# Performance work log

Measured on AMD Instinct MI355X. Metric: run time of the kernel, lower is better.

The kernel has to match this reference:

```python
import jax, jax.numpy as jnp
import numpy as np

K = 3
KK = K * K
PAD = 1          # kernel_size // 2
MAX_SHIFT = 8.0  # bias_range > 0
DEG = 2          # degrees = (2, 2), paon_type 'a'


def setup_inputs() -> dict:
    key = jax.random.key(0)
    ks = jax.random.split(key, 6)
    B, C, O, H, W = 4, 64, 64, 160, 160
    x = jax.random.normal(ks[0], (B, C, H, W), jnp.float32)
    # offset conv is 1x1: weight [2*K*K, C], bias [2*K*K]
    off_w = jax.random.normal(ks[1], (2 * KK, C), jnp.float32) * 0.1
    off_b = jax.random.normal(ks[2], (2 * KK,), jnp.float32) * 0.1
    scale = 1.0 / np.sqrt(C * KK).astype(np.float32)
    w_m = jax.random.normal(ks[3], (DEG * O, C, K, K), jnp.float32) * scale
    w_n = jax.random.normal(ks[4], (DEG * O, C, K, K), jnp.float32) * scale
    w0 = jax.random.normal(ks[5], (O,), jnp.float32) * 0.1
    return {"x": x, "off_w": off_w, "off_b": off_b, "w_m": w_m, "w_n": w_n, "w0": w0}


def _bilinear_sample(x, py, px):
    """x: [B,C,H,W]; py,px: [B,KK,H,W] -> [B,C,KK,H,W]; zero outside bounds."""
    B, C, H, W = x.shape
    xf = x.reshape(B, C, H * W)
    y0 = jnp.floor(py)
    x0 = jnp.floor(px)
    wy = py - y0
    wx = px - x0
    y0i = y0.astype(jnp.int32)
    x0i = x0.astype(jnp.int32)
    out = jnp.zeros((B, C) + py.shape[1:], x.dtype)
    corners = ((0, 0, (1 - wy) * (1 - wx)), (0, 1, (1 - wy) * wx),
               (1, 0, wy * (1 - wx)), (1, 1, wy * wx))
    for dy, dx, wgt in corners:
        yy = y0i + dy
        xx = x0i + dx
        valid = (yy >= 0) & (yy < H) & (xx >= 0) & (xx < W)
        idx = jnp.clip(yy, 0, H - 1) * W + jnp.clip(xx, 0, W - 1)
        g = jax.vmap(lambda f, i: f[:, i])(xf, idx.reshape(B, -1))  # [B,C,KK*H*W]
        out = out + g.reshape(B, C, *py.shape[1:]) * (wgt * valid)[:, None]
    return out


def _after_poly_a(y, ch, o, take_abs):
    # channel reorder + groupwise sum, per PaLaBase.after_poly_a
    order = np.array([(k * ch) % (ch * o) + k // o for k in range(ch * o)])
    y = y[:, order].reshape(y.shape[0], ch, o, *y.shape[2:])
    return jnp.abs(y).sum(2) if take_abs else y.sum(2)


def reference(x, off_w, off_b, w_m, w_n, w0):
    B, C, H, W = x.shape
    O = w0.shape[0]
    # --- DeformOffset: 1x1 conv -> clamp to image -> tanh soft-limit ---
    off_r = jnp.einsum('bchw,oc->bohw', x, off_w) + off_b[None, :, None, None]
    gy = jnp.arange(H, dtype=x.dtype)[None, None, :, None]
    gx = jnp.arange(W, dtype=x.dtype)[None, None, None, :]
    oy = jnp.clip(off_r[:, 0::2], -gy, H - gy)  # [B,KK,H,W] (dy per kernel pos)
    ox = jnp.clip(off_r[:, 1::2], -gx, W - gx)  # [B,KK,H,W] (dx per kernel pos)
    soft = lambda o: jnp.where(jnp.abs(o) >= MAX_SHIFT,
                               MAX_SHIFT * jnp.tanh(o / MAX_SHIFT), o)
    oy, ox = soft(oy), soft(ox)
    # --- deformable sampling grid (stride=1, dilation=1, zero padding) ---
    kidx = jnp.arange(KK)
    kh = (kidx // K).astype(x.dtype)[None, :, None, None]
    kw = (kidx % K).astype(x.dtype)[None, :, None, None]
    base_y = (jnp.arange(H, dtype=x.dtype) - PAD)[None, None, :, None]
    base_x = (jnp.arange(W, dtype=x.dtype) - PAD)[None, None, None, :]
    py = base_y + kh + oy
    px = base_x + kw + ox
    samp = _bilinear_sample(x, py, px)  # [B,C,KK,H,W]
    # --- Pade numerator / denominator convs on the sampled tensor ---
    pm_raw = jnp.einsum('bckhw,ock->bohw', samp, w_m.reshape(DEG * O, C, KK))
    qn_raw = jnp.einsum('bckhw,ock->bohw', samp, w_n.reshape(DEG * O, C, KK))
    pm = _after_poly_a(pm_raw, O, DEG, take_abs=False)
    qn = _after_poly_a(qn_raw, O, DEG, take_abs=True)
    # prepare_for_div_a: (pm + w0, 1 + qn)
    return (pm + w0[None, :, None, None]) / (1.0 + qn)
```

## Files before the change

### kernel.cpp

```cpp
#include <hip/hip_runtime.h>
#include <hip/hip_bf16.h>
#include <hip/hip_fp16.h>

#define Hh 160
#define Ww 160
#define Cc 64
#define HWc 25600
#define Bb 4
#define AST 76

typedef __attribute__((ext_vector_type(8))) short short8;
typedef __attribute__((ext_vector_type(4))) float f32x4;

__device__ __forceinline__ unsigned short f2bf(float f) {
  unsigned int u = __float_as_uint(f);
  unsigned int r = u + 0x7FFFu + ((u >> 16) & 1u);
  return (unsigned short)(r >> 16);
}
__device__ __forceinline__ float bflo(unsigned int u) {
  return __uint_as_float(u << 16);
}
__device__ __forceinline__ float bfhi(unsigned int u) {
  return __uint_as_float(u & 0xffff0000u);
}

__global__ __launch_bounds__(256) void k_prep(
    const float* __restrict__ x, const float* __restrict__ wm,
    const float* __restrict__ wn, const float* __restrict__ ow,
    unsigned short* __restrict__ xT, unsigned short* __restrict__ bf) {
  if (blockIdx.x < 400) {
    __shared__ unsigned short s[64][260];
    int wg = blockIdx.x;
    int b = wg / 100;
    int pix0 = (wg % 100) * 256;
    int l = threadIdx.x & 63, wv = threadIdx.x >> 6;
    const float* xb = x + (size_t)b * Cc * HWc + pix0;
#pragma unroll
    for (int i = 0; i < 16; i++) {
      int c = i * 4 + wv;
      float4 v = *(const float4*)&xb[(size_t)c * HWc + l * 4];
      unsigned int d0 = (unsigned int)f2bf(v.x) | ((unsigned int)f2bf(v.y) << 16);
      unsigned int d1 = (unsigned int)f2bf(v.z) | ((unsigned int)f2bf(v.w) << 16);
      *(uint2*)&s[c][l * 4] = make_uint2(d0, d1);
    }
    __syncthreads();
    int p = threadIdx.x;
    unsigned int w[32];
#pragma unroll
    for (int j = 0; j < 32; j++) {
      unsigned int a = s[2 * j][p];
      unsigned int bb = s[2 * j + 1][p];
      w[j] = a | (bb << 16);
    }
    unsigned short* dst = xT + ((size_t)(b * HWc + pix0 + p)) * 64;
#pragma unroll
    for (int j = 0; j < 8; j++)
      ((uint4*)dst)[j] = make_uint4(w[4 * j], w[4 * j + 1], w[4 * j + 2], w[4 * j + 3]);
  } else {
    int i = (blockIdx.x - 400) * 256 + threadIdx.x;
    if (i < 9 * 2 * 12 * 64 * 8) {
      int j2 = i & 7;
      int lane = (i >> 3) & 63;
      int ntck = i >> 9;
      int nt = ntck % 12;
      int ck = ntck / 12;
      int kk = ck >> 1;
      int chunk = ck & 1;
      int n = nt * 16 + (lane & 15);
      int c = chunk * 32 + (lane >> 4) * 8 + j2;
      float v;
      if (n < 64)
        v = wm[(n * 64 + c) * 9 + kk] + wm[((n + 64) * 64 + c) * 9 + kk];
      else
        v = wn[((n - 64) * 64 + c) * 9 + kk];
      bf[i] = f2bf(v);
    } else if (i < 9 * 2 * 12 * 64 * 8 + 2 * 2 * 64 * 8) {
      int j = i - 9 * 2 * 12 * 64 * 8;
      int j2 = j & 7;
      int lane = (j >> 3) & 63;
      int rest = j >> 9;
      int ntile = rest & 1;
      int chunk = rest >> 1;
      int n = ntile * 16 + (lane & 15);
      int c = chunk * 32 + (lane >> 4) * 8 + j2;
      bf[i] = (n < 18) ? f2bf(ow[n * 64 + c]) : (unsigned short)0;
    }
  }
}

__device__ __forceinline__ void gather2(const char* __restrict__ gbase, uint4 D,
                                        int chB, uint4& c00, uint4& c01,
                                        uint4& c10, uint4& c11, float& w00,
                                        float& w01, float& w10, float& w11) {
  int bb = D.x + chB;
  int dxB = (int)(D.y & 0xffffu);
  int dyB = (int)(D.y >> 16);
  c00 = *(const uint4*)(gbase + bb);
  c01 = *(const uint4*)(gbase + bb + dxB);
  c10 = *(const uint4*)(gbase + bb + dyB);
  c11 = *(const uint4*)(gbase + bb + (dxB + dyB));
  float2 wA = __half22float2(*(const __half2*)&D.z);
  float2 wB = __half22float2(*(const __half2*)&D.w);
  w00 = wA.x; w01 = wA.y; w10 = wB.x; w11 = wB.y;
}

__device__ __forceinline__ void combine_write(unsigned short* Arow,
                                              const uint4& c00, const uint4& c01,
                                              const uint4& c10, const uint4& c11,
                                              float w00, float w01, float w10,
                                              float w11) {
  const unsigned int* a = (const unsigned int*)&c00;
  const unsigned int* b = (const unsigned int*)&c01;
  const unsigned int* c = (const unsigned int*)&c10;
  const unsigned int* d = (const unsigned int*)&c11;
  unsigned int o[4];
#pragma unroll
  for (int j = 0; j < 4; j++) {
    float lo = bflo(a[j]) * w00 + bflo(b[j]) * w01 + bflo(c[j]) * w10 +
               bflo(d[j]) * w11;
    float hi = bfhi(a[j]) * w00 + bfhi(b[j]) * w01 + bfhi(c[j]) * w10 +
               bfhi(d[j]) * w11;
    __hip_bfloat162 hh = __float22bfloat162_rn(make_float2(lo, hi));
    o[j] = *(unsigned int*)&hh;
  }
  *(uint4*)Arow = make_uint4(o[0], o[1], o[2], o[3]);
}

__global__ __launch_bounds__(256, 4) void k_main(
    const unsigned short* __restrict__ xT, const float* __restrict__ w0,
    const float* __restrict__ off_b, const unsigned short* __restrict__ bfrag,
    const unsigned short* __restrict__ obfrag, float* __restrict__ out) {
  __shared__ unsigned short A[2][64 * AST];
  __shared__ uint4 gdesc[576];
  float2* spy = (float2*)&A[0][0];
  const int tid = threadIdx.x;
  const int wg = blockIdx.x;
  const int band = wg & 7;
  const int local = wg >> 3;
  const int b = local / 50;
  const int pix0 = band * 3200 + (local % 50) * 64;
  const int wv = tid >> 6;
  const int l = tid & 63;
  const int lm = l & 15;
  const int quad = l >> 4;
  const int ch8 = l & 7;
  const int pr = l >> 3;
  const int chB = ch8 * 16;

  const unsigned short* xTb = xT + (size_t)b * HWc * 64;
  const char* gbase = (const char*)xTb;

  f32x4 acc[3][4];
  const f32x4 zero = {0.f, 0.f, 0.f, 0.f};
#pragma unroll
  for (int j = 0; j < 3; j++)
#pragma unroll
    for (int pt = 0; pt < 4; pt++) acc[j][pt] = zero;

  {
    f32x4 aO0 = zero, aO1 = zero;
    const unsigned short* xrow = xTb + (size_t)(pix0 + wv * 16 + lm) * 64;
#pragma unroll
    for (int chunk = 0; chunk < 2; chunk++) {
      short8 sb = *(const short8*)(xrow + chunk * 32 + quad * 8);
      short8 wf0 = *(const short8*)&obfrag[((chunk * 2 + 0) * 64 + l) * 8];
      short8 wf1 = *(const short8*)&obfrag[((chunk * 2 + 1) * 64 + l) * 8];
      aO0 = __builtin_amdgcn_mfma_f32_16x16x32_bf16(wf0, sb, aO0, 0, 0, 0);
      aO1 = __builtin_amdgcn_mfma_f32_16x16x32_bf16(wf1, sb, aO1, 0, 0, 0);
    }
    int pix = pix0 + wv * 16 + lm;
    int h = pix / Ww, w = pix % Ww;
    float fh = (float)h, fw = (float)w;
#pragma unroll
    for (int rr = 0; rr < 2; rr++) {
      int n = quad * 4 + 2 * rr;
      int kk = n >> 1;
      float oy = aO0[2 * rr] + off_b[n];
      float ox = aO0[2 * rr + 1] + off_b[n + 1];
      oy = fminf(fmaxf(oy, -fh), 160.0f - fh);
      ox = fminf(fmaxf(ox, -fw), 160.0f - fw);
      if (fabsf(oy) >= 8.0f) oy = 8.0f * tanhf(oy * 0.125f);
      if (fabsf(ox) >= 8.0f) ox = 8.0f * tanhf(ox * 0.125f);
      spy[kk * 64 + wv * 16 + lm] =
          make_float2(fh - 1.0f + (float)(kk / 3) + oy,
                      fw - 1.0f + (float)(kk % 3) + ox);
    }
    if (quad == 0) {
      float oy = aO1[0] + off_b[16];
      float ox = aO1[1] + off_b[17];
      oy = fminf(fmaxf(oy, -fh), 160.0f - fh);
      ox = fminf(fmaxf(ox, -fw), 160.0f - fw);
      if (fabsf(oy) >= 8.0f) oy = 8.0f * tanhf(oy * 0.125f);
      if (fabsf(ox) >= 8.0f) ox = 8.0f * tanhf(ox * 0.125f);
      spy[8 * 64 + wv * 16 + lm] =
          make_float2(fh + 1.0f + oy, fw + 1.0f + ox);
    }
  }
  __syncthreads();

  for (int e = tid; e < 576; e += 256) {
    float2 P = spy[e];
    float py = P.x, pxv = P.y;
    float y0f = floorf(py), x0f = floorf(pxv);
    float wy = py - y0f, wx = pxv - x0f;
    int y0 = (int)y0f, x0 = (int)x0f;
    float vy0 = (y0 >= 0 && y0 < Hh) ? 1.f : 0.f;
    float vy1 = (y0 >= -1 && y0 < Hh - 1) ? 1.f : 0.f;
    float vx0 = (x0 >= 0 && x0 < Ww) ? 1.f : 0.f;
    float vx1 = (x0 >= -1 && x0 < Ww - 1) ? 1.f : 0.f;
    int r0 = min(max(y0, 0), Hh - 1);
    int r1 = min(max(y0 + 1, 0), Hh - 1);
    int c0 = min(max(x0, 0), Ww - 1);
    int c1 = min(max(x0 + 1, 0), Ww - 1);
    float w00 = (1.f - wy) * (1.f - wx) * vy0 * vx0;
    float w01 = (1.f - wy) * wx * vy0 * vx1;
    float w10 = wy * (1.f - wx) * vy1 * vx0;
    float w11 = wy * wx * vy1 * vx1;
    uint4 D;
    D.x = (unsigned int)((r0 * Ww + c0) * 128);
    D.y = (unsigned int)((c1 - c0) * 128) |
          ((unsigned int)((r1 - r0) * Ww * 128) << 16);
    __half2 hA = __floats2half2_rn(w00, w01);
    __half2 hB = __floats2half2_rn(w10, w11);
    D.z = *(unsigned int*)&hA;
    D.w = *(unsigned int*)&hB;
    gdesc[e] = D;
  }
  __syncthreads();

#pragma unroll
  for (int i = 0; i < 2; i++) {
    int pl = wv * 16 + i * 8 + pr;
    uint4 c00, c01, c10, c11;
    float w00, w01, w10, w11;
    gather2(gbase, gdesc[pl], chB, c00, c01, c10, c11, w00, w01, w10, w11);
    combine_write(&A[0][pl * AST + ch8 * 8], c00, c01, c10, c11, w00, w01, w10,
                  w11);
  }
  __syncthreads();

  for (int kk = 0; kk < 9; kk++) {
    const int cur = kk & 1;
    if (kk < 8) {
      uint4 g00[2], g01[2], g10[2], g11[2];
      float W00[2], W01[2], W10[2], W11[2];
#pragma unroll
      for (int i = 0; i < 2; i++) {
        int pl = wv * 16 + i * 8 + pr;
        gather2(gbase, gdesc[(kk + 1) * 64 + pl], chB, g00[i], g01[i], g10[i],
                g11[i], W00[i], W01[i], W10[i], W11[i]);
      }
#pragma unroll
      for (int i = 0; i < 2; i++) {
        int pl = wv * 16 + i * 8 + pr;
        combine_write(&A[cur ^ 1][pl * AST + ch8 * 8], g00[i], g01[i], g10[i],
                      g11[i], W00[i], W01[i], W10[i], W11[i]);
      }
    }
#pragma unroll
    for (int chunk = 0; chunk < 2; chunk++) {
      short8 sfr[4];
#pragma unroll
      for (int pt = 0; pt < 4; pt++)
        sfr[pt] = *(const short8*)&A[cur][(pt * 16 + lm) * AST + chunk * 32 +
                                          quad * 8];
      short8 wfr[3];
#pragma unroll
      for (int j = 0; j < 3; j++) {
        int nt = j * 4 + wv;
        wfr[j] = *(const short8*)&bfrag[((size_t)((kk * 2 + chunk) * 12 + nt) *
                                            64 + l) * 8];
      }
#pragma unroll
      for (int j = 0; j < 3; j++)
#pragma unroll
        for (int pt = 0; pt < 4; pt++)
          acc[j][pt] = __builtin_amdgcn_mfma_f32_16x16x32_bf16(
              wfr[j], sfr[pt], acc[j][pt], 0, 0, 0);
    }
    __syncthreads();
  }

  float w0v[4];
#pragma unroll
  for (int r = 0; r < 4; r++) w0v[r] = w0[wv * 16 + quad * 4 + r];
  float* ob = out + (size_t)b * Cc * HWc + pix0;
#pragma unroll
  for (int pt = 0; pt < 4; pt++) {
#pragma unroll
    for (int r = 0; r < 4; r++) {
      int oc = wv * 16 + quad * 4 + r;
      float pm = acc[0][pt][r] + w0v[r];
      float qn = 1.0f + fabsf(acc[1][pt][r]) + fabsf(acc[2][pt][r]);
      ob[oc * HWc + pt * 16 + lm] = pm / qn;
    }
  }
}

extern "C" void kernel_launch(void* const* d_in, const int* in_sizes, int n_in,
                              void* d_out, int out_size, void* d_ws, size_t ws_size,
                              hipStream_t stream) {
  const float* x = (const float*)d_in[0];
  const float* off_w = (const float*)d_in[1];
  const float* off_b = (const float*)d_in[2];
  const float* w_m = (const float*)d_in[3];
  const float* w_n = (const float*)d_in[4];
  const float* w0 = (const float*)d_in[5];
  float* out = (float*)d_out;

  unsigned short* bfrag = (unsigned short*)d_ws;
  unsigned short* obfrag = (unsigned short*)((char*)d_ws + (size_t)221184);
  unsigned short* xT = (unsigned short*)((char*)d_ws + (size_t)225280);

  hipLaunchKernelGGL(k_prep, dim3(840), dim3(256), 0, stream, x, w_m, w_n,
                     off_w, xT, bfrag);
  hipLaunchKernelGGL(k_main, dim3(1600), dim3(256), 0, stream, xT, w0, off_b,
                     bfrag, obfrag, out);
}
```

Baseline: 133.6 us.

## Gather bilinear samples directly into MFMA fragments with single-wave blocks

Replaces the 4-wave workgroup, which staged bilinear-sampled tiles in double-buffered shared memory, with one-wave blocks covering 32 pixels. Each lane gathers and blends its own MFMA B-fragment straight from global memory into registers, and computes all 12 output tiles with 24 accumulators. This removes the shared-memory staging, bank traffic and per-tap barriers. In exchange each wave reloads the full weight fragments from global/L2 per block, the gather is no longer prefetched a step ahead, and register pressure rises.

```diff
diff --git a/kernel.cpp b/kernel.cpp
--- a/kernel.cpp
+++ b/kernel.cpp
@@ -7,7 +7,6 @@
 #define Cc 64
 #define HWc 25600
 #define Bb 4
-#define AST 76
 
 typedef __attribute__((ext_vector_type(8))) short short8;
 typedef __attribute__((ext_vector_type(4))) float f32x4;
@@ -88,78 +87,65 @@
   }
 }
 
-__device__ __forceinline__ void gather2(const char* __restrict__ gbase, uint4 D,
-                                        int chB, uint4& c00, uint4& c01,
-                                        uint4& c10, uint4& c11, float& w00,
-                                        float& w01, float& w10, float& w11) {
-  int bb = D.x + chB;
+__device__ __forceinline__ short8 gcomb(const char* __restrict__ gbase, uint4 D,
+                                        int off) {
+  int bb = (int)D.x + off;
   int dxB = (int)(D.y & 0xffffu);
   int dyB = (int)(D.y >> 16);
-  c00 = *(const uint4*)(gbase + bb);
-  c01 = *(const uint4*)(gbase + bb + dxB);
-  c10 = *(const uint4*)(gbase + bb + dyB);
-  c11 = *(const uint4*)(gbase + bb + (dxB + dyB));
+  uint4 c00 = *(const uint4*)(gbase + bb);
+  uint4 c01 = *(const uint4*)(gbase + bb + dxB);
+  uint4 c10 = *(const uint4*)(gbase + bb + dyB);
+  uint4 c11 = *(const uint4*)(gbase + bb + dxB + dyB);
   float2 wA = __half22float2(*(const __half2*)&D.z);
   float2 wB = __half22float2(*(const __half2*)&D.w);
-  w00 = wA.x; w01 = wA.y; w10 = wB.x; w11 = wB.y;
-}
-
-__device__ __forceinline__ void combine_write(unsigned short* Arow,
-                                              const uint4& c00, const uint4& c01,
-                                              const uint4& c10, const uint4& c11,
-                                              float w00, float w01, float w10,
-                                              float w11) {
   const unsigned int* a = (const unsigned int*)&c00;
   const unsigned int* b = (const unsigned int*)&c01;
   const unsigned int* c = (const unsigned int*)&c10;
   const unsigned int* d = (const unsigned int*)&c11;
-  unsigned int o[4];
+  uint4 o;
+  unsigned int* op = (unsigned int*)&o;
 #pragma unroll
   for (int j = 0; j < 4; j++) {
-    float lo = bflo(a[j]) * w00 + bflo(b[j]) * w01 + bflo(c[j]) * w10 +
-               bflo(d[j]) * w11;
-    float hi = bfhi(a[j]) * w00 + bfhi(b[j]) * w01 + bfhi(c[j]) * w10 +
-               bfhi(d[j]) * w11;
+    float lo = bflo(a[j]) * wA.x + bflo(b[j]) * wA.y + bflo(c[j]) * wB.x +
+               bflo(d[j]) * wB.y;
+    float hi = bfhi(a[j]) * wA.x + bfhi(b[j]) * wA.y + bfhi(c[j]) * wB.x +
+               bfhi(d[j]) * wB.y;
     __hip_bfloat162 hh = __float22bfloat162_rn(make_float2(lo, hi));
-    o[j] = *(unsigned int*)&hh;
-  }
-  *(uint4*)Arow = make_uint4(o[0], o[1], o[2], o[3]);
-}
-
-__global__ __launch_bounds__(256, 4) void k_main(
+    op[j] = *(unsigned int*)&hh;
+  }
+  return *(short8*)&o;
+}
+
+__global__ __launch_bounds__(64, 3) void k_main(
     const unsigned short* __restrict__ xT, const float* __restrict__ w0,
     const float* __restrict__ off_b, const unsigned short* __restrict__ bfrag,
     const unsigned short* __restrict__ obfrag, float* __restrict__ out) {
-  __shared__ unsigned short A[2][64 * AST];
-  __shared__ uint4 gdesc[576];
-  float2* spy = (float2*)&A[0][0];
-  const int tid = threadIdx.x;
+  __shared__ uint4 gdesc[288];
+  __shared__ float2 spy[288];
+  const int l = threadIdx.x;
   const int wg = blockIdx.x;
   const int band = wg & 7;
   const int local = wg >> 3;
-  const int b = local / 50;
-  const int pix0 = band * 3200 + (local % 50) * 64;
-  const int wv = tid >> 6;
-  const int l = tid & 63;
+  const int b = local / 100;
+  const int pix0 = band * 3200 + (local % 100) * 32;
   const int lm = l & 15;
   const int quad = l >> 4;
-  const int ch8 = l & 7;
-  const int pr = l >> 3;
-  const int chB = ch8 * 16;
 
   const unsigned short* xTb = xT + (size_t)b * HWc * 64;
   const char* gbase = (const char*)xTb;
 
-  f32x4 acc[3][4];
+  f32x4 acc[12][2];
   const f32x4 zero = {0.f, 0.f, 0.f, 0.f};
 #pragma unroll
-  for (int j = 0; j < 3; j++)
-#pragma unroll
-    for (int pt = 0; pt < 4; pt++) acc[j][pt] = zero;
-
-  {
+  for (int nt = 0; nt < 12; nt++) {
+    acc[nt][0] = zero;
+    acc[nt][1] = zero;
+  }
+
+#pragma unroll
+  for (int g = 0; g < 2; g++) {
     f32x4 aO0 = zero, aO1 = zero;
-    const unsigned short* xrow = xTb + (size_t)(pix0 + wv * 16 + lm) * 64;
+    const unsigned short* xrow = xTb + (size_t)(pix0 + g * 16 + lm) * 64;
 #pragma unroll
     for (int chunk = 0; chunk < 2; chunk++) {
       short8 sb = *(const short8*)(xrow + chunk * 32 + quad * 8);
@@ -168,7 +154,7 @@
       aO0 = __builtin_amdgcn_mfma_f32_16x16x32_bf16(wf0, sb, aO0, 0, 0, 0);
       aO1 = __builtin_amdgcn_mfma_f32_16x16x32_bf16(wf1, sb, aO1, 0, 0, 0);
     }
-    int pix = pix0 + wv * 16 + lm;
+    int pix = pix0 + g * 16 + lm;
     int h = pix / Ww, w = pix % Ww;
     float fh = (float)h, fw = (float)w;
 #pragma unroll
@@ -181,7 +167,7 @@
       ox = fminf(fmaxf(ox, -fw), 160.0f - fw);
       if (fabsf(oy) >= 8.0f) oy = 8.0f * tanhf(oy * 0.125f);
       if (fabsf(ox) >= 8.0f) ox = 8.0f * tanhf(ox * 0.125f);
-      spy[kk * 64 + wv * 16 + lm] =
+      spy[kk * 32 + g * 16 + lm] =
           make_float2(fh - 1.0f + (float)(kk / 3) + oy,
                       fw - 1.0f + (float)(kk % 3) + ox);
     }
@@ -192,13 +178,13 @@
       ox = fminf(fmaxf(ox, -fw), 160.0f - fw);
       if (fabsf(oy) >= 8.0f) oy = 8.0f * tanhf(oy * 0.125f);
       if (fabsf(ox) >= 8.0f) ox = 8.0f * tanhf(ox * 0.125f);
-      spy[8 * 64 + wv * 16 + lm] =
+      spy[8 * 32 + g * 16 + lm] =
           make_float2(fh + 1.0f + oy, fw + 1.0f + ox);
     }
   }
   __syncthreads();
 
-  for (int e = tid; e < 576; e += 256) {
+  for (int e = l; e < 288; e += 64) {
     float2 P = spy[e];
     float py = P.x, pxv = P.y;
     float y0f = floorf(py), x0f = floorf(pxv);
@@ -228,71 +214,41 @@
   }
   __syncthreads();
 
-#pragma unroll
-  for (int i = 0; i < 2; i++) {
-    int pl = wv * 16 + i * 8 + pr;
-    uint4 c00, c01, c10, c11;
-    float w00, w01, w10, w11;
-    gather2(gbase, gdesc[pl], chB, c00, c01, c10, c11, w00, w01, w10, w11);
-    combine_write(&A[0][pl * AST + ch8 * 8], c00, c01, c10, c11, w00, w01, w10,
-                  w11);
-  }
-  __syncthreads();
-
   for (int kk = 0; kk < 9; kk++) {
-    const int cur = kk & 1;
-    if (kk < 8) {
-      uint4 g00[2], g01[2], g10[2], g11[2];
-      float W00[2], W01[2], W10[2], W11[2];
-#pragma unroll
-      for (int i = 0; i < 2; i++) {
-        int pl = wv * 16 + i * 8 + pr;
-        gather2(gbase, gdesc[(kk + 1) * 64 + pl], chB, g00[i], g01[i], g10[i],
-                g11[i], W00[i], W01[i], W10[i], W11[i]);
+    uint4 D0 = gdesc[kk * 32 + lm];
+    uint4 D1 = gdesc[kk * 32 + 16 + lm];
+    const unsigned short* wbase = bfrag + (size_t)(kk * 2) * 12 * 512;
+#pragma unroll
+    for (int chunk = 0; chunk < 2; chunk++) {
+      const int off = chunk * 64 + quad * 16;
+      short8 sfr0 = gcomb(gbase, D0, off);
+      short8 sfr1 = gcomb(gbase, D1, off);
+      const unsigned short* wck = wbase + (size_t)chunk * 12 * 512 + l * 8;
+#pragma unroll
+      for (int nt = 0; nt < 12; nt++) {
+        short8 wfr = *(const short8*)(wck + nt * 512);
+        acc[nt][0] =
+            __builtin_amdgcn_mfma_f32_16x16x32_bf16(wfr, sfr0, acc[nt][0], 0, 0, 0);
+        acc[nt][1] =
+            __builtin_amdgcn_mfma_f32_16x16x32_bf16(wfr, sfr1, acc[nt][1], 0, 0, 0);
       }
-#pragma unroll
-      for (int i = 0; i < 2; i++) {
-        int pl = wv * 16 + i * 8 + pr;
-        combine_write(&A[cur ^ 1][pl * AST + ch8 * 8], g00[i], g01[i], g10[i],
-                      g11[i], W00[i], W01[i], W10[i], W11[i]);
+    }
+  }
+
+  float* ob = out + (size_t)b * Cc * HWc + pix0;
+#pragma unroll
+  for (int nt = 0; nt < 4; nt++) {
+#pragma unroll
+    for (int r = 0; r < 4; r++) {
+      int oc = nt * 16 + quad * 4 + r;
+      float w0v = w0[oc];
+#pragma unroll
+      for (int g = 0; g < 2; g++) {
+        float pm = acc[nt][g][r] + w0v;
+        float qn =
+            1.0f + fabsf(acc[nt + 4][g][r]) + fabsf(acc[nt + 8][g][r]);
+        ob[(size_t)oc * HWc + g * 16 + lm] = pm / qn;
       }
-    }
-#pragma unroll
-    for (int chunk = 0; chunk < 2; chunk++) {
-      short8 sfr[4];
-#pragma unroll
-      for (int pt = 0; pt < 4; pt++)
-        sfr[pt] = *(const short8*)&A[cur][(pt * 16 + lm) * AST + chunk * 32 +
-                                          quad * 8];
-      short8 wfr[3];
-#pragma unroll
-      for (int j = 0; j < 3; j++) {
-        int nt = j * 4 + wv;
-        wfr[j] = *(const short8*)&bfrag[((size_t)((kk * 2 + chunk) * 12 + nt) *
-                                            64 + l) * 8];
-      }
-#pragma unroll
-      for (int j = 0; j < 3; j++)
-#pragma unroll
-        for (int pt = 0; pt < 4; pt++)
-          acc[j][pt] = __builtin_amdgcn_mfma_f32_16x16x32_bf16(
-              wfr[j], sfr[pt], acc[j][pt], 0, 0, 0);
-    }
-    __syncthreads();
-  }
-
-  float w0v[4];
-#pragma unroll
-  for (int r = 0; r < 4; r++) w0v[r] = w0[wv * 16 + quad * 4 + r];
-  float* ob = out + (size_t)b * Cc * HWc + pix0;
-#pragma unroll
-  for (int pt = 0; pt < 4; pt++) {
-#pragma unroll
-    for (int r = 0; r < 4; r++) {
-      int oc = wv * 16 + quad * 4 + r;
-      float pm = acc[0][pt][r] + w0v[r];
-      float qn = 1.0f + fabsf(acc[1][pt][r]) + fabsf(acc[2][pt][r]);
-      ob[oc * HWc + pt * 16 + lm] = pm / qn;
     }
   }
 }
@@ -314,6 +270,6 @@
 
   hipLaunchKernelGGL(k_prep, dim3(840), dim3(256), 0, stream, x, w_m, w_n,
                      off_w, xT, bfrag);
-  hipLaunchKernelGGL(k_main, dim3(1600), dim3(256), 0, stream, xT, w0, off_b,
+  hipLaunchKernelGGL(k_main, dim3(3200), dim3(64), 0, stream, xT, w0, off_b,
                      bfrag, obfrag, out);
 }
```

New measurement: 384.5 us. 188% more time.

## Switch gather/MFMA path to fp16 with packed half2 bilinear combine, overlap gathers with MFMA

Applied to the files above, without the earlier changes.

Converts the staged input and weights from bf16 to fp16 so the bilinear combine can use packed half2 FMAs instead of unpacking to fp32, and uses the f16 MFMA variant. It also reorders the pipeline so the next tap's global gathers are issued before the MFMAs and combined/written afterwards, letting gather latency overlap matrix math. fp16 narrows range relative to bf16, and combining in half precision adds rounding error. Holding the gathered registers across the MFMAs raises register pressure.

```diff
diff --git a/kernel.cpp b/kernel.cpp
--- a/kernel.cpp
+++ b/kernel.cpp
@@ -9,19 +9,12 @@
 #define Bb 4
 #define AST 76
 
-typedef __attribute__((ext_vector_type(8))) short short8;
+typedef __attribute__((ext_vector_type(8))) _Float16 half8;
 typedef __attribute__((ext_vector_type(4))) float f32x4;
 
-__device__ __forceinline__ unsigned short f2bf(float f) {
-  unsigned int u = __float_as_uint(f);
-  unsigned int r = u + 0x7FFFu + ((u >> 16) & 1u);
-  return (unsigned short)(r >> 16);
-}
-__device__ __forceinline__ float bflo(unsigned int u) {
-  return __uint_as_float(u << 16);
-}
-__device__ __forceinline__ float bfhi(unsigned int u) {
-  return __uint_as_float(u & 0xffff0000u);
+__device__ __forceinline__ unsigned int f2h2u(float a, float b) {
+  __half2 h = __floats2half2_rn(a, b);
+  return *(unsigned int*)&h;
 }
 
 __global__ __launch_bounds__(256) void k_prep(
@@ -39,9 +32,7 @@
     for (int i = 0; i < 16; i++) {
       int c = i * 4 + wv;
       float4 v = *(const float4*)&xb[(size_t)c * HWc + l * 4];
-      unsigned int d0 = (unsigned int)f2bf(v.x) | ((unsigned int)f2bf(v.y) << 16);
-      unsigned int d1 = (unsigned int)f2bf(v.z) | ((unsigned int)f2bf(v.w) << 16);
-      *(uint2*)&s[c][l * 4] = make_uint2(d0, d1);
+      *(uint2*)&s[c][l * 4] = make_uint2(f2h2u(v.x, v.y), f2h2u(v.z, v.w));
     }
     __syncthreads();
     int p = threadIdx.x;
@@ -50,7 +41,7 @@
     for (int j = 0; j < 32; j++) {
       unsigned int a = s[2 * j][p];
       unsigned int bb = s[2 * j + 1][p];
-      w[j] = a | (bb << 16);
+      w[j] = (a & 0xffffu) | (bb << 16);
     }
     unsigned short* dst = xT + ((size_t)(b * HWc + pix0 + p)) * 64;
 #pragma unroll
@@ -73,7 +64,8 @@
         v = wm[(n * 64 + c) * 9 + kk] + wm[((n + 64) * 64 + c) * 9 + kk];
       else
         v = wn[((n - 64) * 64 + c) * 9 + kk];
-      bf[i] = f2bf(v);
+      __half hv = __float2half_rn(v);
+      bf[i] = *(unsigned short*)&hv;
     } else if (i < 9 * 2 * 12 * 64 * 8 + 2 * 2 * 64 * 8) {
       int j = i - 9 * 2 * 12 * 64 * 8;
       int j2 = j & 7;
@@ -83,32 +75,41 @@
       int chunk = rest >> 1;
       int n = ntile * 16 + (lane & 15);
       int c = chunk * 32 + (lane >> 4) * 8 + j2;
-      bf[i] = (n < 18) ? f2bf(ow[n * 64 + c]) : (unsigned short)0;
-    }
-  }
-}
-
-__device__ __forceinline__ void gather2(const char* __restrict__ gbase, uint4 D,
-                                        int chB, uint4& c00, uint4& c01,
-                                        uint4& c10, uint4& c11, float& w00,
-                                        float& w01, float& w10, float& w11) {
-  int bb = D.x + chB;
+      if (n < 18) {
+        __half hv = __float2half_rn(ow[n * 64 + c]);
+        bf[i] = *(unsigned short*)&hv;
+      } else {
+        bf[i] = 0;
+      }
+    }
+  }
+}
+
+__device__ __forceinline__ void gather2h(const char* __restrict__ gbase, uint4 D,
+                                         int chB, uint4& c00, uint4& c01,
+                                         uint4& c10, uint4& c11, __half2& W00,
+                                         __half2& W01, __half2& W10,
+                                         __half2& W11) {
+  int bb = (int)D.x + chB;
   int dxB = (int)(D.y & 0xffffu);
   int dyB = (int)(D.y >> 16);
   c00 = *(const uint4*)(gbase + bb);
   c01 = *(const uint4*)(gbase + bb + dxB);
   c10 = *(const uint4*)(gbase + bb + dyB);
-  c11 = *(const uint4*)(gbase + bb + (dxB + dyB));
-  float2 wA = __half22float2(*(const __half2*)&D.z);
-  float2 wB = __half22float2(*(const __half2*)&D.w);
-  w00 = wA.x; w01 = wA.y; w10 = wB.x; w11 = wB.y;
+  c11 = *(const uint4*)(gbase + bb + dxB + dyB);
+  __half2 wz = *(const __half2*)&D.z;
+  __half2 ww = *(const __half2*)&D.w;
+  W00 = __half2half2(__low2half(wz));
+  W01 = __half2half2(__high2half(wz));
+  W10 = __half2half2(__low2half(ww));
+  W11 = __half2half2(__high2half(ww));
 }
 
 __device__ __forceinline__ void combine_write(unsigned short* Arow,
                                               const uint4& c00, const uint4& c01,
                                               const uint4& c10, const uint4& c11,
-                                              float w00, float w01, float w10,
-                                              float w11) {
+                                              __half2 W00, __half2 W01,
+                                              __half2 W10, __half2 W11) {
   const unsigned int* a = (const unsigned int*)&c00;
   const unsigned int* b = (const unsigned int*)&c01;
   const unsigned int* c = (const unsigned int*)&c10;
@@ -116,12 +117,13 @@
   unsigned int o[4];
 #pragma unroll
   for (int j = 0; j < 4; j++) {
-    float lo = bflo(a[j]) * w00 + bflo(b[j]) * w01 + bflo(c[j]) * w10 +
-               bflo(d[j]) * w11;
-    float hi = bfhi(a[j]) * w00 + bfhi(b[j]) * w01 + bfhi(c[j]) * w10 +
-               bfhi(d[j]) * w11;
-    __hip_bfloat162 hh = __float22bfloat162_rn(make_float2(lo, hi));
-    o[j] = *(unsigned int*)&hh;
+    __half2 ha = *(const __half2*)&a[j];
+    __half2 hb = *(const __half2*)&b[j];
+    __half2 hc = *(const __half2*)&c[j];
+    __half2 hd = *(const __half2*)&d[j];
+    __half2 r = __hfma2(ha, W00,
+                        __hfma2(hb, W01, __hfma2(hc, W10, __hmul2(hd, W11))));
+    o[j] = *(unsigned int*)&r;
   }
   *(uint4*)Arow = make_uint4(o[0], o[1], o[2], o[3]);
 }
@@ -162,11 +164,11 @@
     const unsigned short* xrow = xTb + (size_t)(pix0 + wv * 16 + lm) * 64;
 #pragma unroll
     for (int chunk = 0; chunk < 2; chunk++) {
-      short8 sb = *(const short8*)(xrow + chunk * 32 + quad * 8);
-      short8 wf0 = *(const short8*)&obfrag[((chunk * 2 + 0) * 64 + l) * 8];
-      short8 wf1 = *(const short8*)&obfrag[((chunk * 2 + 1) * 64 + l) * 8];
-      aO0 = __builtin_amdgcn_mfma_f32_16x16x32_bf16(wf0, sb, aO0, 0, 0, 0);
-      aO1 = __builtin_amdgcn_mfma_f32_16x16x32_bf16(wf1, sb, aO1, 0, 0, 0);
+      half8 sb = *(const half8*)(xrow + chunk * 32 + quad * 8);
+      half8 wf0 = *(const half8*)&obfrag[((chunk * 2 + 0) * 64 + l) * 8];
+      half8 wf1 = *(const half8*)&obfrag[((chunk * 2 + 1) * 64 + l) * 8];
+      aO0 = __builtin_amdgcn_mfma_f32_16x16x32_f16(wf0, sb, aO0, 0, 0, 0);
+      aO1 = __builtin_amdgcn_mfma_f32_16x16x32_f16(wf1, sb, aO1, 0, 0, 0);
     }
     int pix = pix0 + wv * 16 + lm;
     int h = pix / Ww, w = pix % Ww;
@@ -220,10 +222,8 @@
     D.x = (unsigned int)((r0 * Ww + c0) * 128);
     D.y = (unsigned int)((c1 - c0) * 128) |
           ((unsigned int)((r1 - r0) * Ww * 128) << 16);
-    __half2 hA = __floats2half2_rn(w00, w01);
-    __half2 hB = __floats2half2_rn(w10, w11);
-    D.z = *(unsigned int*)&hA;
-    D.w = *(unsigned int*)&hB;
+    D.z = f2h2u(w00, w01);
+    D.w = f2h2u(w10, w11);
     gdesc[e] = D;
   }
   __syncthreads();
@@ -232,51 +232,53 @@
   for (int i = 0; i < 2; i++) {
     int pl = wv * 16 + i * 8 + pr;
     uint4 c00, c01, c10, c11;
-    float w00, w01, w10, w11;
-    gather2(gbase, gdesc[pl], chB, c00, c01, c10, c11, w00, w01, w10, w11);
-    combine_write(&A[0][pl * AST + ch8 * 8], c00, c01, c10, c11, w00, w01, w10,
-                  w11);
+    __half2 W00, W01, W10, W11;
+    gather2h(gbase, gdesc[pl], chB, c00, c01, c10, c11, W00, W01, W10, W11);
+    combine_write(&A[0][pl * AST + ch8 * 8], c00, c01, c10, c11, W00, W01, W10,
+                  W11);
   }
   __syncthreads();
 
   for (int kk = 0; kk < 9; kk++) {
     const int cur = kk & 1;
+    uint4 g00[2], g01[2], g10[2], g11[2];
+    __half2 W00[2], W01[2], W10[2], W11[2];
     if (kk < 8) {
-      uint4 g00[2], g01[2], g10[2], g11[2];
-      float W00[2], W01[2], W10[2], W11[2];
 #pragma unroll
       for (int i = 0; i < 2; i++) {
         int pl = wv * 16 + i * 8 + pr;
-        gather2(gbase, gdesc[(kk + 1) * 64 + pl], chB, g00[i], g01[i], g10[i],
-                g11[i], W00[i], W01[i], W10[i], W11[i]);
+        gather2h(gbase, gdesc[(kk + 1) * 64 + pl], chB, g00[i], g01[i], g10[i],
+                 g11[i], W00[i], W01[i], W10[i], W11[i]);
       }
+    }
+#pragma unroll
+    for (int chunk = 0; chunk < 2; chunk++) {
+      half8 sfr[4];
+#pragma unroll
+      for (int pt = 0; pt < 4; pt++)
+        sfr[pt] = *(const half8*)&A[cur][(pt * 16 + lm) * AST + chunk * 32 +
+                                         quad * 8];
+      half8 wfr[3];
+#pragma unroll
+      for (int j = 0; j < 3; j++) {
+        int nt = j * 4 + wv;
+        wfr[j] = *(const half8*)&bfrag[((size_t)((kk * 2 + chunk) * 12 + nt) *
+                                           64 + l) * 8];
+      }
+#pragma unroll
+      for (int j = 0; j < 3; j++)
+#pragma unroll
+        for (int pt = 0; pt < 4; pt++)
+          acc[j][pt] = __builtin_amdgcn_mfma_f32_16x16x32_f16(
+              wfr[j], sfr[pt], acc[j][pt], 0, 0, 0);
+    }
+    if (kk < 8) {
 #pragma unroll
       for (int i = 0; i < 2; i++) {
         int pl = wv * 16 + i * 8 + pr;
         combine_write(&A[cur ^ 1][pl * AST + ch8 * 8], g00[i], g01[i], g10[i],
                       g11[i], W00[i], W01[i], W10[i], W11[i]);
       }
-    }
-#pragma unroll
-    for (int chunk = 0; chunk < 2; chunk++) {
-      short8 sfr[4];
-#pragma unroll
-      for (int pt = 0; pt < 4; pt++)
-        sfr[pt] = *(const short8*)&A[cur][(pt * 16 + lm) * AST + chunk * 32 +
-                                          quad * 8];
-      short8 wfr[3];
-#pragma unroll
-      for (int j = 0; j < 3; j++) {
-        int nt = j * 4 + wv;
-        wfr[j] = *(const short8*)&bfrag[((size_t)((kk * 2 + chunk) * 12 + nt) *
-                                            64 + l) * 8];
-      }
-#pragma unroll
-      for (int j = 0; j < 3; j++)
-#pragma unroll
-        for (int pt = 0; pt < 4; pt++)
-          acc[j][pt] = __builtin_amdgcn_mfma_f32_16x16x32_bf16(
-              wfr[j], sfr[pt], acc[j][pt], 0, 0, 0);
     }
     __syncthreads();
   }
```

After: 126.6 us. 1.06x faster.
